# Kernel tuning notes

Measured on AMD Instinct MI355X. Metric: run time of the kernel, lower is better.

Reference implementation:

```python
import jax, jax.numpy as jnp
from jax import lax
import numpy as np

B, C, O, H, W = 4, 64, 64, 128, 128


def setup_inputs() -> dict:
    key = jax.random.key(0)
    ks = jax.random.split(key, 3)
    x = jax.random.normal(ks[0], (B, C, H, W), dtype=jnp.float32)
    # small offset-conv weights so learned offsets stay in a realistic +-few-pixel range
    offset_w = jax.random.normal(ks[1], (27, C, 3, 3), dtype=jnp.float32) * 0.01
    offset_b = jnp.zeros((27,), dtype=jnp.float32)
    dcn_w = jax.random.normal(ks[2], (O, C, 3, 3), dtype=jnp.float32) * (1.0 / np.sqrt(C * 9))
    dcn_b = jnp.zeros((O,), dtype=jnp.float32)
    gamma = jnp.ones((O,), dtype=jnp.float32)
    beta = jnp.zeros((O,), dtype=jnp.float32)
    return {"x": x, "offset_w": offset_w, "offset_b": offset_b,
            "dcn_w": dcn_w, "dcn_b": dcn_b, "gamma": gamma, "beta": beta}


def _bilinear_sample(img, y, x):
    """img: [B,C,H,W]; y,x: [B,K,H,W] fractional coords. Returns [B,C,K,H,W].
    Out-of-range corners contribute 0 (DCNv2 semantics)."""
    Bs, Cs, Hs, Ws = img.shape
    flat = img.reshape(Bs, Cs, Hs * Ws)
    y0 = jnp.floor(y)
    x0 = jnp.floor(x)
    wy = y - y0
    wx = x - x0

    def gather(yi, xi):
        valid = (yi >= 0) & (yi <= Hs - 1) & (xi >= 0) & (xi <= Ws - 1)
        yc = jnp.clip(yi, 0, Hs - 1).astype(jnp.int32)
        xc = jnp.clip(xi, 0, Ws - 1).astype(jnp.int32)
        idx = (yc * Ws + xc).reshape(Bs, -1)  # [B, K*H*W]
        v = jax.vmap(lambda f, i: jnp.take(f, i, axis=1))(flat, idx)  # [B,C,K*H*W]
        v = v.reshape(Bs, Cs, *y.shape[1:])
        return v * valid[:, None].astype(img.dtype)

    out = jnp.zeros((Bs, Cs) + y.shape[1:], dtype=img.dtype)
    for dy, dx in ((0, 0), (0, 1), (1, 0), (1, 1)):
        w = (wy if dy else 1.0 - wy) * (wx if dx else 1.0 - wx)
        out = out + gather(y0 + dy, x0 + dx) * w[:, None]
    return out


def reference(x, offset_w, offset_b, dcn_w, dcn_b, gamma, beta):
    Bs, Cs, Hs, Ws = x.shape
    Os = dcn_w.shape[0]
    # offset-predicting 3x3 conv, stride 1, pad 1
    om = lax.conv_general_dilated(
        x, offset_w, window_strides=(1, 1), padding=((1, 1), (1, 1)),
        dimension_numbers=("NCHW", "OIHW", "NCHW")) + offset_b[None, :, None, None]
    off_x, off_y, mask = jnp.split(om, 3, axis=1)  # each [B,9,H,W]
    mask = jax.nn.sigmoid(mask)

    # base sampling grid: p0 + kernel tap offset (stride 1, pad 1, dil 1)
    ky, kx = jnp.meshgrid(jnp.arange(3), jnp.arange(3), indexing="ij")
    kyf = ky.reshape(9).astype(x.dtype)
    kxf = kx.reshape(9).astype(x.dtype)
    hh = jnp.arange(Hs, dtype=x.dtype)
    ww = jnp.arange(Ws, dtype=x.dtype)
    py = hh[None, None, :, None] - 1.0 + kyf[None, :, None, None] + off_y  # [B,9,H,W]
    px = ww[None, None, None, :] - 1.0 + kxf[None, :, None, None] + off_x  # [B,9,H,W]

    sampled = _bilinear_sample(x, py, px)          # [B,C,9,H,W]
    sampled = sampled * mask[:, None]              # sigmoid modulation
    out = jnp.einsum("bckhw,ock->bohw", sampled, dcn_w.reshape(Os, Cs, 9))
    out = out + dcn_b[None, :, None, None]

    # BatchNorm (training-mode batch stats) + ReLU
    mu = out.mean(axis=(0, 2, 3), keepdims=True)
    var = out.var(axis=(0, 2, 3), keepdims=True)
    out = (out - mu) * lax.rsqrt(var + 1e-5)
    out = out * gamma[None, :, None, None] + beta[None, :, None, None]
    return jax.nn.relu(out)
```

## Files before the change

### kernel.cpp

```cpp
#include <hip/hip_runtime.h>
#include <math.h>

#define Hh 128
#define Ww 128
#define HW (Hh*Ww)
#define Bn 4
#define Cn 64
#define On 64
#define KP 200
#define OMP 66
#define NBLK 1024

typedef __attribute__((ext_vector_type(8))) short bf16x8;
typedef __attribute__((ext_vector_type(4))) float f32x4;
typedef __attribute__((ext_vector_type(4))) unsigned short u16x4;

static __device__ __forceinline__ unsigned short f2bf(float f) {
    unsigned u = __builtin_bit_cast(unsigned, f);
    u += 0x7FFFu + ((u >> 16) & 1u);
    return (unsigned short)(u >> 16);
}
static __device__ __forceinline__ short f2h(float f) {
    _Float16 h = (_Float16)f;
    return __builtin_bit_cast(short, h);
}
static __device__ __forceinline__ float h2f(short s) {
    return (float)__builtin_bit_cast(_Float16, s);
}

#define XTB_BYTES   ((size_t)Bn*HW*64*2)
#define CONV_BYTES  ((size_t)Bn*On*HW*4)
#define PART_BYTES  ((size_t)128*NBLK*4)

__global__ __launch_bounds__(256) void prep_k(
    const float* __restrict__ x,  const float* __restrict__ ow,
    const float* __restrict__ dw, unsigned* __restrict__ xtb,
    short* __restrict__ owT,      short* __restrict__ dwT)
{
    int blk = blockIdx.x;
    int t = threadIdx.x;
    if (blk < 512) {
        int b = blk >> 7, h = blk & 127;
        __shared__ float sT[64 * 133];
        const float* xp = x + (size_t)b * Cn * HW + (size_t)h * Ww;
#pragma unroll
        for (int it = 0; it < 32; ++it) {
            int idx = t + 256 * it;
            int c = idx >> 7, w = idx & 127;
            sT[c * 133 + w] = xp[(size_t)c * HW + w];
        }
        __syncthreads();
        unsigned* op = xtb + (size_t)blk * Ww * 32;
#pragma unroll
        for (int it = 0; it < 16; ++it) {
            int idx = t + 256 * it;
            int w = idx >> 5, cp = idx & 31;
            unsigned lo = f2bf(sT[(2 * cp) * 133 + w]);
            unsigned hi = f2bf(sT[(2 * cp + 1) * 133 + w]);
            op[(size_t)w * 32 + cp] = lo | (hi << 16);
        }
    } else {
        int u = (blk - 512) * 4 + (t >> 6);
        int c = t & 63;
        if (u < 288) {
            int o = u / 9, kk = u % 9;
            float v = (o < 27) ? ow[(size_t)o * 576 + c * 9 + kk] : 0.0f;
            owT[(size_t)u * 64 + c] = (short)f2bf(v);
        } else {
            int u2 = u - 288;
            int o = u2 / 9, kk = u2 % 9;
            dwT[(size_t)u2 * 64 + c] = (short)f2bf(dw[(size_t)o * 576 + c * 9 + kk]);
        }
    }
}

__global__ __launch_bounds__(256) void dcn_fused_k(
    const unsigned* __restrict__ xtb, const short* __restrict__ owT,
    const float* __restrict__ ob,     const short* __restrict__ dwT,
    float* __restrict__ conv,         float* __restrict__ part)
{
    int raw  = blockIdx.x;
    int blk  = ((raw & 7) << 7) | (raw >> 3);
    int half = blk & 1;
    int h    = (blk >> 1) & 127;
    int b    = blk >> 8;
    int px0  = half * 64;
    int t    = threadIdx.x;
    int lane = t & 63;
    int quad = lane >> 4;
    int l15  = lane & 15;
    int hl   = lane >> 5;
    int cl   = lane & 31;
    int w_s  = __builtin_amdgcn_readfirstlane(t >> 6);

    __shared__ __align__(16) short sA[64 * KP];
    __shared__ __align__(16) unsigned short prepQ[576 * 4];
    __shared__ __align__(16) unsigned short prepC[576];
    short* sOMh = sA;

    const unsigned* xbd = xtb + (size_t)b * HW * 32;
    unsigned* sAd = (unsigned*)sA;

    int nt_o = w_s & 1;
    int mh   = w_s >> 1;
    int o_ow = nt_o * 16 + l15;
    f32x4 oacc[2] = {{0,0,0,0},{0,0,0,0}};

    for (int ck = 0; ck < 3; ++ck) {
#pragma unroll 4
        for (int pr = 0; pr < 24; ++pr) {
            int pair = pr * 4 + w_s;
            int kkl = pair >> 5, px2 = pair & 31;
            int px = px2 * 2 + hl;
            int yy = h + ck - 1;
            int xx = px0 + px + kkl - 1;
            bool valid = ((unsigned)yy < (unsigned)Hh) && ((unsigned)xx < (unsigned)Ww);
            unsigned v = valid ? xbd[(((size_t)yy << 7) + xx) * 32 + cl] : 0u;
            sAd[px * 100 + kkl * 32 + cl] = v;
        }
        __syncthreads();
#pragma unroll
        for (int ks = 0; ks < 6; ++ks) {
            int kk = ck * 3 + (ks >> 1);
            bf16x8 bfr = *(const bf16x8*)&owT[((size_t)o_ow * 9 + kk) * 64
                                             + (ks & 1) * 32 + quad * 8];
#pragma unroll
            for (int m2 = 0; m2 < 2; ++m2) {
                bf16x8 a = *(const bf16x8*)&sA[(mh * 32 + m2 * 16 + l15) * KP
                                               + ks * 32 + quad * 8];
                oacc[m2] = __builtin_amdgcn_mfma_f32_16x16x32_bf16(a, bfr, oacc[m2], 0, 0, 0);
            }
        }
        __syncthreads();
    }
    if (o_ow < 27) {
        float bias = ob[o_ow];
#pragma unroll
        for (int m2 = 0; m2 < 2; ++m2) {
            int pxb = (mh * 2 + m2) * 16 + quad * 4;
#pragma unroll
            for (int r = 0; r < 4; ++r)
                sOMh[o_ow * OMP + pxb + r] = f2h(oacc[m2][r] + bias);
        }
    }
    __syncthreads();

#pragma unroll
    for (int i = 0; i < 3; ++i) {
        int u = t + 256 * i;
        if (u < 576) {
            int kk = u >> 6, px = u & 63;
            float ox = h2f((short)sOMh[kk * OMP + px]);
            float oy = h2f((short)sOMh[(9 + kk) * OMP + px]);
            float mr = h2f((short)sOMh[(18 + kk) * OMP + px]);
            float m  = 1.0f / (1.0f + __expf(-mr));
            float py  = (float)(h - 1 + (kk / 3)) + oy;
            float pxf = (float)(px0 + px - 1 + (kk % 3)) + ox;
            float y0f = floorf(py), x0f = floorf(pxf);
            int y0 = (int)y0f, x0 = (int)x0f;
            float wy = py - y0f, wx = pxf - x0f;
            int yb = min(max(y0, 0), Hh - 2);
            int xb = min(max(x0, 0), Ww - 2);
            float wr0 = (yb == y0) ? (1.0f - wy) : ((yb     == y0 + 1) ? wy : 0.0f);
            float wr1 = (yb == y0) ? wy          : ((yb + 1 == y0    ) ? (1.0f - wy) : 0.0f);
            float wc0 = (xb == x0) ? (1.0f - wx) : ((xb     == x0 + 1) ? wx : 0.0f);
            float wc1 = (xb == x0) ? wx          : ((xb + 1 == x0    ) ? (1.0f - wx) : 0.0f);
            wr0 *= m; wr1 *= m;
            prepQ[u * 4 + 0] = (unsigned short)(yb * Ww + xb);
            prepQ[u * 4 + 1] = (unsigned short)f2h(wr0 * wc0);
            prepQ[u * 4 + 2] = (unsigned short)f2h(wr0 * wc1);
            prepQ[u * 4 + 3] = (unsigned short)f2h(wr1 * wc0);
            prepC[u]         = (unsigned short)f2h(wr1 * wc1);
        }
    }
    __syncthreads();

    int o_dw = w_s * 16 + l15;
    f32x4 acc[4] = {{0,0,0,0},{0,0,0,0},{0,0,0,0},{0,0,0,0}};

    for (int ck = 0; ck < 3; ++ck) {
#pragma unroll 4
        for (int uu = 0; uu < 24; ++uu) {
            int unit = (uu * 4 + w_s) * 2 + hl;
            int kkl = unit >> 6, px = unit & 63;
            int u = ck * 192 + unit;
            u16x4 q = *(const u16x4*)&prepQ[u * 4];
            float w00 = h2f((short)q[1]);
            float w01 = h2f((short)q[2]);
            float w10 = h2f((short)q[3]);
            float w11 = h2f((short)prepC[u]);
            const unsigned* p0 = xbd + (size_t)q[0] * 32 + cl;
            unsigned d00 = p0[0];
            unsigned d01 = p0[32];
            unsigned d10 = p0[4096];
            unsigned d11 = p0[4128];
            float v0 = w00 * __builtin_bit_cast(float, d00 << 16)
                     + w01 * __builtin_bit_cast(float, d01 << 16)
                     + w10 * __builtin_bit_cast(float, d10 << 16)
                     + w11 * __builtin_bit_cast(float, d11 << 16);
            float v1 = w00 * __builtin_bit_cast(float, d00 & 0xFFFF0000u)
                     + w01 * __builtin_bit_cast(float, d01 & 0xFFFF0000u)
                     + w10 * __builtin_bit_cast(float, d10 & 0xFFFF0000u)
                     + w11 * __builtin_bit_cast(float, d11 & 0xFFFF0000u);
            unsigned pk;
            asm("v_cvt_pk_bf16_f32 %0, %1, %2" : "=v"(pk) : "v"(v0), "v"(v1));
            sAd[px * 100 + kkl * 32 + cl] = pk;
        }
        __syncthreads();
#pragma unroll
        for (int ks = 0; ks < 6; ++ks) {
            int kk = ck * 3 + (ks >> 1);
            bf16x8 bfr = *(const bf16x8*)&dwT[((size_t)o_dw * 9 + kk) * 64
                                              + (ks & 1) * 32 + quad * 8];
#pragma unroll
            for (int mt = 0; mt < 4; ++mt) {
                bf16x8 a = *(const bf16x8*)&sA[(mt * 16 + l15) * KP
                                               + ks * 32 + quad * 8];
                acc[mt] = __builtin_amdgcn_mfma_f32_16x16x32_bf16(a, bfr, acc[mt], 0, 0, 0);
            }
        }
        __syncthreads();
    }

#pragma unroll
    for (int mt = 0; mt < 4; ++mt) {
        size_t idx = ((size_t)b * On + o_dw) * HW + (size_t)h * Ww + px0 + mt * 16 + quad * 4;
        *(f32x4*)(conv + idx) = acc[mt];
    }
    float s1 = 0.0f, s2 = 0.0f;
#pragma unroll
    for (int mt = 0; mt < 4; ++mt) {
#pragma unroll
        for (int r = 0; r < 4; ++r) {
            float v = acc[mt][r];
            s1 += v;
            s2 += v * v;
        }
    }
    s1 += __shfl_down(s1, 32, 64);  s2 += __shfl_down(s2, 32, 64);
    s1 += __shfl_down(s1, 16, 64);  s2 += __shfl_down(s2, 16, 64);
    if (lane < 16) {
        part[(size_t)o_dw * NBLK + blk]        = s1;
        part[(size_t)(64 + o_dw) * NBLK + blk] = s2;
    }
}

__global__ __launch_bounds__(256) void bnstats_k(
    const float* __restrict__ part, const float* __restrict__ gamma,
    const float* __restrict__ beta, const float* __restrict__ conv,
    float* __restrict__ out)
{
    int idx = blockIdx.x;
    int o  = idx & 63;
    int bq = idx >> 6;
    int t = threadIdx.x;
    float s1 = 0.0f, s2 = 0.0f;
#pragma unroll
    for (int i = 0; i < NBLK / 256; ++i) {
        int j = t + 256 * i;
        s1 += part[(size_t)o * NBLK + j];
        s2 += part[(size_t)(64 + o) * NBLK + j];
    }
#pragma unroll
    for (int off = 32; off > 0; off >>= 1) {
        s1 += __shfl_down(s1, off, 64);
        s2 += __shfl_down(s2, off, 64);
    }
    __shared__ float r1[4], r2[4];
    __shared__ float sc_s, sh_s;
    if ((t & 63) == 0) { r1[t >> 6] = s1; r2[t >> 6] = s2; }
    __syncthreads();
    if (t == 0) {
        float S1 = r1[0] + r1[1] + r1[2] + r1[3];
        float S2 = r2[0] + r2[1] + r2[2] + r2[3];
        float n = (float)(Bn * HW);
        float mu = S1 / n;
        float var = S2 / n - mu * mu;
        float sc = gamma[o] * rsqrtf(var + 1e-5f);
        sc_s = sc;
        sh_s = beta[o] - mu * sc;
    }
    __syncthreads();
    float sc = sc_s, sh = sh_s;
    size_t base = (((size_t)(bq >> 2) * On + o) * HW + (size_t)(bq & 3) * 4096) / 4;
    const float4* cv = (const float4*)conv + base;
    float4* ov = (float4*)out + base;
#pragma unroll
    for (int i = 0; i < 4; ++i) {
        float4 v = cv[t + 256 * i];
        v.x = fmaxf(v.x * sc + sh, 0.0f);
        v.y = fmaxf(v.y * sc + sh, 0.0f);
        v.z = fmaxf(v.z * sc + sh, 0.0f);
        v.w = fmaxf(v.w * sc + sh, 0.0f);
        ov[t + 256 * i] = v;
    }
}

extern "C" void kernel_launch(void* const* d_in, const int* in_sizes, int n_in,
                              void* d_out, int out_size, void* d_ws, size_t ws_size,
                              hipStream_t stream)
{
    const float* x     = (const float*)d_in[0];
    const float* ow    = (const float*)d_in[1];
    const float* ob    = (const float*)d_in[2];
    const float* dw    = (const float*)d_in[3];
    const float* gamma = (const float*)d_in[5];
    const float* beta  = (const float*)d_in[6];

    char* wsb = (char*)d_ws;
    unsigned* xtb = (unsigned*)wsb;
    float* conv = (float*)(wsb + XTB_BYTES);
    float* part = (float*)(wsb + XTB_BYTES + CONV_BYTES);
    short* owT  = (short*)(wsb + XTB_BYTES + CONV_BYTES + PART_BYTES + 512);
    short* dwT  = owT + 288 * 64;

    prep_k     <<<dim3(728),  dim3(256), 0, stream>>>(x, ow, dw, xtb, owT, dwT);
    dcn_fused_k<<<dim3(NBLK), dim3(256), 0, stream>>>(xtb, owT, ob, dwT, conv, part);
    bnstats_k  <<<dim3(1024), dim3(256), 0, stream>>>(part, gamma, beta, conv, (float*)d_out);
}
```

Measured before the change: 136.8 us.

## Partition work per-wave by pixel rows to remove block barriers in fused DCN kernel

```diff
diff --git a/kernel.cpp b/kernel.cpp
--- a/kernel.cpp
+++ b/kernel.cpp
@@ -92,64 +92,63 @@
     int hl   = lane >> 5;
     int cl   = lane & 31;
     int w_s  = __builtin_amdgcn_readfirstlane(t >> 6);
+    int pxq  = w_s << 4;
 
     __shared__ __align__(16) short sA[64 * KP];
+    __shared__ __align__(16) short sOMh[27 * OMP + 12];
     __shared__ __align__(16) unsigned short prepQ[576 * 4];
     __shared__ __align__(16) unsigned short prepC[576];
-    short* sOMh = sA;
+    __shared__ float sredA[4][64], sredB[4][64];
 
     const unsigned* xbd = xtb + (size_t)b * HW * 32;
     unsigned* sAd = (unsigned*)sA;
 
-    int nt_o = w_s & 1;
-    int mh   = w_s >> 1;
-    int o_ow = nt_o * 16 + l15;
     f32x4 oacc[2] = {{0,0,0,0},{0,0,0,0}};
 
     for (int ck = 0; ck < 3; ++ck) {
+        int yy = h + ck - 1;
+        bool rowok = ((unsigned)yy < (unsigned)Hh);
 #pragma unroll 4
-        for (int pr = 0; pr < 24; ++pr) {
-            int pair = pr * 4 + w_s;
-            int kkl = pair >> 5, px2 = pair & 31;
-            int px = px2 * 2 + hl;
-            int yy = h + ck - 1;
+        for (int it = 0; it < 24; ++it) {
+            int unit = it * 2 + hl;
+            int kkl = unit >> 4, pxl = unit & 15;
+            int px = pxq + pxl;
             int xx = px0 + px + kkl - 1;
-            bool valid = ((unsigned)yy < (unsigned)Hh) && ((unsigned)xx < (unsigned)Ww);
+            bool valid = rowok && ((unsigned)xx < (unsigned)Ww);
             unsigned v = valid ? xbd[(((size_t)yy << 7) + xx) * 32 + cl] : 0u;
             sAd[px * 100 + kkl * 32 + cl] = v;
         }
-        __syncthreads();
+        asm volatile("s_waitcnt lgkmcnt(0)" ::: "memory");
 #pragma unroll
         for (int ks = 0; ks < 6; ++ks) {
             int kk = ck * 3 + (ks >> 1);
-            bf16x8 bfr = *(const bf16x8*)&owT[((size_t)o_ow * 9 + kk) * 64
-                                             + (ks & 1) * 32 + quad * 8];
-#pragma unroll
-            for (int m2 = 0; m2 < 2; ++m2) {
-                bf16x8 a = *(const bf16x8*)&sA[(mh * 32 + m2 * 16 + l15) * KP
-                                               + ks * 32 + quad * 8];
-                oacc[m2] = __builtin_amdgcn_mfma_f32_16x16x32_bf16(a, bfr, oacc[m2], 0, 0, 0);
+            bf16x8 a = *(const bf16x8*)&sA[(pxq + l15) * KP + ks * 32 + quad * 8];
+#pragma unroll
+            for (int nt = 0; nt < 2; ++nt) {
+                bf16x8 bfr = *(const bf16x8*)&owT[((size_t)(nt * 16 + l15) * 9 + kk) * 64
+                                                  + (ks & 1) * 32 + quad * 8];
+                oacc[nt] = __builtin_amdgcn_mfma_f32_16x16x32_bf16(a, bfr, oacc[nt], 0, 0, 0);
             }
         }
-        __syncthreads();
-    }
-    if (o_ow < 27) {
-        float bias = ob[o_ow];
-#pragma unroll
-        for (int m2 = 0; m2 < 2; ++m2) {
-            int pxb = (mh * 2 + m2) * 16 + quad * 4;
+    }
+#pragma unroll
+    for (int nt = 0; nt < 2; ++nt) {
+        int o = nt * 16 + l15;
+        if (o < 27) {
+            float bias = ob[o];
 #pragma unroll
             for (int r = 0; r < 4; ++r)
-                sOMh[o_ow * OMP + pxb + r] = f2h(oacc[m2][r] + bias);
-        }
-    }
-    __syncthreads();
-
-#pragma unroll
-    for (int i = 0; i < 3; ++i) {
-        int u = t + 256 * i;
-        if (u < 576) {
-            int kk = u >> 6, px = u & 63;
+                sOMh[o * OMP + pxq + (quad << 2) + r] = f2h(oacc[nt][r] + bias);
+        }
+    }
+    asm volatile("s_waitcnt lgkmcnt(0)" ::: "memory");
+
+#pragma unroll
+    for (int j = 0; j < 3; ++j) {
+        int unit = j * 64 + lane;
+        if (unit < 144) {
+            int kk = unit >> 4, pxl = unit & 15;
+            int px = pxq + pxl;
             float ox = h2f((short)sOMh[kk * OMP + px]);
             float oy = h2f((short)sOMh[(9 + kk) * OMP + px]);
             float mr = h2f((short)sOMh[(18 + kk) * OMP + px]);
@@ -166,29 +165,30 @@
             float wc0 = (xb == x0) ? (1.0f - wx) : ((xb     == x0 + 1) ? wx : 0.0f);
             float wc1 = (xb == x0) ? wx          : ((xb + 1 == x0    ) ? (1.0f - wx) : 0.0f);
             wr0 *= m; wr1 *= m;
-            prepQ[u * 4 + 0] = (unsigned short)(yb * Ww + xb);
-            prepQ[u * 4 + 1] = (unsigned short)f2h(wr0 * wc0);
-            prepQ[u * 4 + 2] = (unsigned short)f2h(wr0 * wc1);
-            prepQ[u * 4 + 3] = (unsigned short)f2h(wr1 * wc0);
-            prepC[u]         = (unsigned short)f2h(wr1 * wc1);
-        }
-    }
-    __syncthreads();
-
-    int o_dw = w_s * 16 + l15;
+            int uG = (kk << 6) + px;
+            prepQ[uG * 4 + 0] = (unsigned short)(yb * Ww + xb);
+            prepQ[uG * 4 + 1] = (unsigned short)f2h(wr0 * wc0);
+            prepQ[uG * 4 + 2] = (unsigned short)f2h(wr0 * wc1);
+            prepQ[uG * 4 + 3] = (unsigned short)f2h(wr1 * wc0);
+            prepC[uG]         = (unsigned short)f2h(wr1 * wc1);
+        }
+    }
+    asm volatile("s_waitcnt lgkmcnt(0)" ::: "memory");
+
     f32x4 acc[4] = {{0,0,0,0},{0,0,0,0},{0,0,0,0},{0,0,0,0}};
 
     for (int ck = 0; ck < 3; ++ck) {
 #pragma unroll 4
-        for (int uu = 0; uu < 24; ++uu) {
-            int unit = (uu * 4 + w_s) * 2 + hl;
-            int kkl = unit >> 6, px = unit & 63;
-            int u = ck * 192 + unit;
-            u16x4 q = *(const u16x4*)&prepQ[u * 4];
+        for (int it = 0; it < 24; ++it) {
+            int unit = it * 2 + hl;
+            int kkl = unit >> 4, pxl = unit & 15;
+            int px = pxq + pxl;
+            int uG = (ck * 3 + kkl) * 64 + px;
+            u16x4 q = *(const u16x4*)&prepQ[uG * 4];
             float w00 = h2f((short)q[1]);
             float w01 = h2f((short)q[2]);
             float w10 = h2f((short)q[3]);
-            float w11 = h2f((short)prepC[u]);
+            float w11 = h2f((short)prepC[uG]);
             const unsigned* p0 = xbd + (size_t)q[0] * 32 + cl;
             unsigned d00 = p0[0];
             unsigned d01 = p0[32];
@@ -206,42 +206,44 @@
             asm("v_cvt_pk_bf16_f32 %0, %1, %2" : "=v"(pk) : "v"(v0), "v"(v1));
             sAd[px * 100 + kkl * 32 + cl] = pk;
         }
-        __syncthreads();
+        asm volatile("s_waitcnt lgkmcnt(0)" ::: "memory");
 #pragma unroll
         for (int ks = 0; ks < 6; ++ks) {
             int kk = ck * 3 + (ks >> 1);
-            bf16x8 bfr = *(const bf16x8*)&dwT[((size_t)o_dw * 9 + kk) * 64
-                                              + (ks & 1) * 32 + quad * 8];
-#pragma unroll
-            for (int mt = 0; mt < 4; ++mt) {
-                bf16x8 a = *(const bf16x8*)&sA[(mt * 16 + l15) * KP
-                                               + ks * 32 + quad * 8];
-                acc[mt] = __builtin_amdgcn_mfma_f32_16x16x32_bf16(a, bfr, acc[mt], 0, 0, 0);
+            bf16x8 a = *(const bf16x8*)&sA[(pxq + l15) * KP + ks * 32 + quad * 8];
+#pragma unroll
+            for (int nt = 0; nt < 4; ++nt) {
+                bf16x8 bfr = *(const bf16x8*)&dwT[((size_t)(nt * 16 + l15) * 9 + kk) * 64
+                                                  + (ks & 1) * 32 + quad * 8];
+                acc[nt] = __builtin_amdgcn_mfma_f32_16x16x32_bf16(a, bfr, acc[nt], 0, 0, 0);
             }
         }
-        __syncthreads();
-    }
-
-#pragma unroll
-    for (int mt = 0; mt < 4; ++mt) {
-        size_t idx = ((size_t)b * On + o_dw) * HW + (size_t)h * Ww + px0 + mt * 16 + quad * 4;
-        *(f32x4*)(conv + idx) = acc[mt];
-    }
-    float s1 = 0.0f, s2 = 0.0f;
-#pragma unroll
-    for (int mt = 0; mt < 4; ++mt) {
-#pragma unroll
-        for (int r = 0; r < 4; ++r) {
-            float v = acc[mt][r];
-            s1 += v;
-            s2 += v * v;
-        }
-    }
-    s1 += __shfl_down(s1, 32, 64);  s2 += __shfl_down(s2, 32, 64);
-    s1 += __shfl_down(s1, 16, 64);  s2 += __shfl_down(s2, 16, 64);
-    if (lane < 16) {
-        part[(size_t)o_dw * NBLK + blk]        = s1;
-        part[(size_t)(64 + o_dw) * NBLK + blk] = s2;
+    }
+
+#pragma unroll
+    for (int nt = 0; nt < 4; ++nt) {
+        int o = nt * 16 + l15;
+        size_t idx = ((size_t)b * On + o) * HW + (size_t)h * Ww + px0 + pxq + (quad << 2);
+        *(f32x4*)(conv + idx) = acc[nt];
+    }
+#pragma unroll
+    for (int nt = 0; nt < 4; ++nt) {
+        float s1 = acc[nt][0] + acc[nt][1] + acc[nt][2] + acc[nt][3];
+        float s2 = acc[nt][0] * acc[nt][0] + acc[nt][1] * acc[nt][1]
+                 + acc[nt][2] * acc[nt][2] + acc[nt][3] * acc[nt][3];
+        s1 += __shfl_down(s1, 32, 64);  s2 += __shfl_down(s2, 32, 64);
+        s1 += __shfl_down(s1, 16, 64);  s2 += __shfl_down(s2, 16, 64);
+        if (lane < 16) {
+            sredA[w_s][nt * 16 + lane] = s1;
+            sredB[w_s][nt * 16 + lane] = s2;
+        }
+    }
+    __syncthreads();
+    if (t < 64) {
+        float S1 = sredA[0][t] + sredA[1][t] + sredA[2][t] + sredA[3][t];
+        float S2 = sredB[0][t] + sredB[1][t] + sredB[2][t] + sredB[3][t];
+        part[(size_t)t * NBLK + blk]        = S1;
+        part[(size_t)(64 + t) * NBLK + blk] = S2;
     }
 }
 
```

Result: slower. 162.6 us (+18.8%).
